# Performance work log

Measured on AMD Instinct MI355X. Metric: run time of the kernel, lower is better.

## Reference

```python
import jax, jax.numpy as jnp
import numpy as np
import math

N_HEAD = 16
N_KV_HEAD = 4
HEAD_DIM = 128
ROTARY_DIM = 128
ROTARY_BASE = 10000
N_CTX = 2048


def _sin_cos(rotary_dim, n_ctx, base):
    pos = np.arange(n_ctx, dtype=np.float32)
    dim = np.arange(rotary_dim // 2, dtype=np.float32)
    freq = base ** (dim / (rotary_dim / 2))
    freq = np.concatenate([freq, freq])  # non-adjacent-pairs layout
    angles = pos[:, None] / freq[None, :]
    return jnp.asarray(np.sin(angles)), jnp.asarray(np.cos(angles))


def _rotate_half(x):
    n = x.shape[-1] // 2
    return jnp.concatenate([-x[..., n:], x[..., :n]], axis=-1)


def setup_inputs() -> dict:
    key = jax.random.key(0)
    ks = jax.random.split(key, 5)
    B, T, C = 2, 2048, 2048
    kv = N_KV_HEAD * HEAD_DIM
    s = 0.02
    return {
        "x": jax.random.normal(ks[0], (B, T, C), jnp.float32),
        "Wq": jax.random.normal(ks[1], (C, C), jnp.float32) * s,
        "Wk": jax.random.normal(ks[2], (kv, C), jnp.float32) * s,
        "Wv": jax.random.normal(ks[3], (kv, C), jnp.float32) * s,
        "Wo": jax.random.normal(ks[4], (C, C), jnp.float32) * s,
    }


def reference(x, Wq, Wk, Wv, Wo):
    B, T, C = x.shape
    q = (x @ Wq.T).reshape(B, T, N_HEAD, HEAD_DIM).transpose(0, 2, 1, 3)    # bhtd
    k = (x @ Wk.T).reshape(B, T, N_KV_HEAD, HEAD_DIM).transpose(0, 2, 1, 3)
    v = (x @ Wv.T).reshape(B, T, N_KV_HEAD, HEAD_DIM).transpose(0, 2, 1, 3)

    sin, cos = _sin_cos(ROTARY_DIM, N_CTX, ROTARY_BASE)
    pos = jnp.arange(T)
    c = cos[pos][None, None, :, :]  # 1,1,T,rot
    s = sin[pos][None, None, :, :]
    q = q * c + _rotate_half(q) * s
    k = k * c + _rotate_half(k) * s

    rep = N_HEAD // N_KV_HEAD
    k = jnp.repeat(k, rep, axis=1)
    v = jnp.repeat(v, rep, axis=1)

    scale = 1.0 / math.sqrt(HEAD_DIM)
    att = jnp.einsum("bhqd,bhkd->bhqk", q, k) * scale
    causal = jnp.tril(jnp.ones((T, T), bool))
    att = jnp.where(causal[None, None], att, -jnp.inf)
    att = jax.nn.softmax(att, axis=-1)
    y = jnp.einsum("bhqk,bhkd->bhqd", att, v)
    y = y.transpose(0, 2, 1, 3).reshape(B, T, C)
    return y @ Wo.T
```

## Files before the change

### kernel.cpp

```cpp
#include <hip/hip_runtime.h>
#include <hip/hip_bf16.h>

typedef float f32x4 __attribute__((ext_vector_type(4)));
typedef float f32x16 __attribute__((ext_vector_type(16)));
typedef short s16x8 __attribute__((ext_vector_type(8)));
typedef short s16x4 __attribute__((ext_vector_type(4)));

__device__ __forceinline__ short f2bf(float f) {
  union { float f; unsigned u; } v; v.f = f;
  unsigned r = v.u + 0x7fffu + ((v.u >> 16) & 1u);
  return (short)(r >> 16);
}
__device__ __forceinline__ float bf2f(short s) {
  union { unsigned u; float f; } v; v.u = ((unsigned)(unsigned short)s) << 16;
  return v.f;
}
__device__ __forceinline__ unsigned cvtpk(float lo, float hi) {
  unsigned r;
  asm("v_cvt_pk_bf16_f32 %0, %1, %2" : "=v"(r) : "v"(lo), "v"(hi));
  return r;
}

__device__ __forceinline__ void gload_lds16(const short* g, short* l) {
  __builtin_amdgcn_global_load_lds(
      (const __attribute__((address_space(1))) void*)g,
      (__attribute__((address_space(3))) void*)l, 16, 0, 0);
}

__global__ __launch_bounds__(256) void k_f2bf(const float* __restrict__ in,
                                              short* __restrict__ out, int n8) {
  int i = blockIdx.x * 256 + threadIdx.x;
  if (i >= n8) return;
  const float4* p = (const float4*)in + (size_t)i * 2;
  float4 a = p[0], b = p[1];
  s16x8 o;
  o[0] = f2bf(a.x); o[1] = f2bf(a.y); o[2] = f2bf(a.z); o[3] = f2bf(a.w);
  o[4] = f2bf(b.x); o[5] = f2bf(b.y); o[6] = f2bf(b.z); o[7] = f2bf(b.w);
  *(s16x8*)(out + (size_t)i * 8) = o;
}

template <int MODE>
__global__ __launch_bounds__(256) void k_gemm_bt(const short* __restrict__ A,
                                                 const short* __restrict__ Bw,
                                                 void* __restrict__ C,
                                                 void* __restrict__ C2,
                                                 void* __restrict__ C3,
                                                 int M, int N, int K) {
  __shared__ __align__(16) short As[128 * 64];
  __shared__ __align__(16) short Bs[128 * 64];
  const int tid = threadIdx.x;
  const int w = tid >> 6, lane = tid & 63;
  const int wm = w >> 1, wn = w & 1;
  const int bm = blockIdx.y, bn = blockIdx.x;
  const int l15 = lane & 15, l4 = lane >> 4;

  f32x4 acc[4][4] = {};

  const int nk = K >> 6;
  for (int kt = 0; kt < nk; ++kt) {
    __syncthreads();
#pragma unroll
    for (int it = 0; it < 4; ++it) {
      int p = it * 256 + tid;
      int p0 = it * 256 + w * 64;
      int r = p >> 3, j = p & 7;
      int jsrc = j ^ (r & 7);
      gload_lds16(A + (size_t)(bm * 128 + r) * K + kt * 64 + jsrc * 8, &As[p0 * 8]);
      gload_lds16(Bw + (size_t)(bn * 128 + r) * K + kt * 64 + jsrc * 8, &Bs[p0 * 8]);
    }
    __syncthreads();
#pragma unroll
    for (int kk = 0; kk < 2; ++kk) {
      s16x8 af[4], bf[4];
      const int jj = kk * 4 + l4;
#pragma unroll
      for (int mi = 0; mi < 4; ++mi) {
        int r = wm * 64 + mi * 16 + l15;
        af[mi] = *(const s16x8*)&As[(r * 8 + (jj ^ (r & 7))) * 8];
      }
#pragma unroll
      for (int ni = 0; ni < 4; ++ni) {
        int r = wn * 64 + ni * 16 + l15;
        bf[ni] = *(const s16x8*)&Bs[(r * 8 + (jj ^ (r & 7))) * 8];
      }
      __builtin_amdgcn_s_setprio(1);
#pragma unroll
      for (int mi = 0; mi < 4; ++mi)
#pragma unroll
        for (int ni = 0; ni < 4; ++ni)
          acc[mi][ni] = __builtin_amdgcn_mfma_f32_16x16x32_bf16(
              af[mi], bf[ni], acc[mi][ni], 0, 0, 0);
      __builtin_amdgcn_s_setprio(0);
    }
  }

#pragma unroll
  for (int mi = 0; mi < 4; ++mi) {
#pragma unroll
    for (int ni = 0; ni < 4; ++ni) {
      int row0 = bm * 128 + wm * 64 + mi * 16 + l4 * 4;
      int col = bn * 128 + wn * 64 + ni * 16 + l15;
      if (MODE == 1) {
        float* Cf = (float*)C;
#pragma unroll
        for (int r2 = 0; r2 < 4; ++r2)
          Cf[(size_t)(row0 + r2) * N + col] = acc[mi][ni][r2];
      } else {
        if (col < 2048) {
          short* Qo = (short*)C;
#pragma unroll
          for (int r2 = 0; r2 < 4; ++r2)
            Qo[(size_t)(row0 + r2) * 2048 + col] = f2bf(acc[mi][ni][r2]);
        } else if (col < 2560) {
          short* Ko = (short*)C2;
#pragma unroll
          for (int r2 = 0; r2 < 4; ++r2)
            Ko[(size_t)(row0 + r2) * 512 + (col - 2048)] = f2bf(acc[mi][ni][r2]);
        } else {
          short* Vo = (short*)C3;
          int b = row0 >> 11, t0 = row0 & 2047;
          s16x4 pk;
#pragma unroll
          for (int r2 = 0; r2 < 4; ++r2) pk[r2] = f2bf(acc[mi][ni][r2]);
          *(s16x4*)&Vo[(size_t)b * 1048576 + (size_t)(col - 2560) * 2048 + t0] = pk;
        }
      }
    }
  }
}

__global__ __launch_bounds__(256) void k_rope(short* __restrict__ X, int shift,
                                              int rowstride, float mul) {
  int idx = blockIdx.x * 256 + threadIdx.x;
  int row = idx >> shift;
  int rem = idx & ((1 << shift) - 1);
  int h = rem >> 6, d = rem & 63;
  int t = row & 2047;
  float inv = exp2f(-(float)d * (13.287712379549449f / 64.f));
  float ang = (float)t * inv;
  float s, c;
  sincosf(ang, &s, &c);
  size_t base = (size_t)row * rowstride + h * 128 + d;
  float q0 = bf2f(X[base]), q1 = bf2f(X[base + 64]);
  X[base] = f2bf((q0 * c - q1 * s) * mul);
  X[base + 64] = f2bf((q1 * c + q0 * s) * mul);
}

__global__ __launch_bounds__(256, 2) void k_attn3(const short* __restrict__ Q,
                                                  const short* __restrict__ Kb,
                                                  const short* __restrict__ Vt,
                                                  short* __restrict__ Y) {
  __shared__ __align__(16) short Ks[2][64 * 128];
  __shared__ __align__(16) short Vs[2][128 * 64];

  const int tid = threadIdx.x;
  const int w = tid >> 6, lane = tid & 63;
  const int l31 = lane & 31, h5 = lane >> 5;
  const int qx = blockIdx.x, h = blockIdx.y, b = blockIdx.z;
  const int qi = b ? (15 - qx) : qx;
  const int kh = h >> 2;

  s16x8 qf[8];
  const int qrow_local = qi * 128 + w * 32 + l31;
  const size_t qrow = (size_t)(b * 2048 + qrow_local);
#pragma unroll
  for (int f = 0; f < 8; ++f)
    qf[f] = *(const s16x8*)(Q + qrow * 2048 + h * 128 + f * 16 + h5 * 8);

  f32x16 oacc[4] = {};
  float m = -1e30f, l = 0.f;

  const int jmax = 2 * qi + 1;

  auto stage = [&](int buf, int j) {
#pragma unroll
    for (int it = 0; it < 4; ++it) {
      int p = it * 256 + tid;
      int p0 = it * 256 + w * 64;
      int r = p >> 4, c = p & 15;
      int csrc = (c - r) & 15;
      gload_lds16(Kb + (size_t)(b * 2048 + j * 64 + r) * 512 + kh * 128 + csrc * 8,
                  &Ks[buf][p0 * 8]);
    }
#pragma unroll
    for (int it = 0; it < 4; ++it) {
      int p = it * 256 + tid;
      int p0 = it * 256 + w * 64;
      int r = p >> 3, c = p & 7;
      int csrc = (c - r) & 7;
      gload_lds16(Vt + (size_t)b * 1048576 + (size_t)(kh * 128 + r) * 2048 +
                      j * 64 + csrc * 8,
                  &Vs[buf][p0 * 8]);
    }
  };

  stage(0, 0);
  __syncthreads();

  for (int j = 0; j <= jmax; ++j) {
    const int cur = j & 1;
    if (j < jmax) stage(cur ^ 1, j + 1);

    f32x16 sa0 = {}, sa1 = {};
    __builtin_amdgcn_s_setprio(1);
#pragma unroll
    for (int f = 0; f < 8; ++f) {
      int c = f * 2 + h5;
      int r0 = l31, r1 = 32 + l31;
      s16x8 k0 = *(const s16x8*)&Ks[cur][(r0 * 16 + ((c + r0) & 15)) * 8];
      s16x8 k1 = *(const s16x8*)&Ks[cur][(r1 * 16 + ((c + r1) & 15)) * 8];
      sa0 = __builtin_amdgcn_mfma_f32_32x32x16_bf16(k0, qf[f], sa0, 0, 0, 0);
      sa1 = __builtin_amdgcn_mfma_f32_32x32x16_bf16(k1, qf[f], sa1, 0, 0, 0);
    }
    __builtin_amdgcn_s_setprio(0);

    if (j >= 2 * qi) {
      const int kv0 = j * 64;
#pragma unroll
      for (int rg = 0; rg < 16; ++rg) {
        int krow = (rg & 3) + 8 * (rg >> 2) + 4 * h5;
        if (kv0 + krow > qrow_local) sa0[rg] = -3.0e38f;
        if (kv0 + 32 + krow > qrow_local) sa1[rg] = -3.0e38f;
      }
    }

    float mx[16];
#pragma unroll
    for (int i = 0; i < 16; ++i) mx[i] = fmaxf(sa0[i], sa1[i]);
#pragma unroll
    for (int stp = 8; stp > 0; stp >>= 1)
#pragma unroll
      for (int i = 0; i < stp; ++i) mx[i] = fmaxf(mx[i], mx[i + stp]);
    float pm = fmaxf(mx[0], __shfl_xor(mx[0], 32));

    if (!__all(pm - m <= 8.f)) {
      float mn = fmaxf(m, pm);
      float al = exp2f(m - mn);
      m = mn;
      l *= al;
#pragma unroll
      for (int d = 0; d < 4; ++d)
#pragma unroll
        for (int i = 0; i < 16; ++i) oacc[d][i] *= al;
    }

    float sm[16];
#pragma unroll
    for (int i = 0; i < 16; ++i) {
      float e0 = exp2f(sa0[i] - m);
      float e1 = exp2f(sa1[i] - m);
      sa0[i] = e0; sa1[i] = e1;
      sm[i] = e0 + e1;
    }
#pragma unroll
    for (int stp = 8; stp > 0; stp >>= 1)
#pragma unroll
      for (int i = 0; i < stp; ++i) sm[i] += sm[i + stp];
    l += sm[0] + __shfl_xor(sm[0], 32);

    unsigned u0[8], u1[8];
#pragma unroll
    for (int g = 0; g < 4; ++g) {
      u0[2 * g]     = cvtpk(sa0[4 * g + 0], sa0[4 * g + 1]);
      u0[2 * g + 1] = cvtpk(sa0[4 * g + 2], sa0[4 * g + 3]);
      u1[2 * g]     = cvtpk(sa1[4 * g + 0], sa1[4 * g + 1]);
      u1[2 * g + 1] = cvtpk(sa1[4 * g + 2], sa1[4 * g + 3]);
    }
    unsigned pu0[8], pu1[8];
#pragma unroll
    for (int g2 = 0; g2 < 8; ++g2) {
      pu0[g2] = __shfl_xor(u0[g2], 32);
      pu1[g2] = __shfl_xor(u1[g2], 32);
    }
    s16x8 pb[4];
#pragma unroll
    for (int fp = 0; fp < 4; ++fp) {
      int j0a = (4 * fp) & 6, j0b = (4 * fp + 2) & 6;
      union { unsigned uu[4]; s16x8 v; } cv;
      if (fp < 2) {
        cv.uu[0] = h5 ? pu0[j0b]     : u0[j0a];
        cv.uu[1] = h5 ? pu0[j0b + 1] : u0[j0a + 1];
        cv.uu[2] = h5 ? u0[j0b]      : pu0[j0a];
        cv.uu[3] = h5 ? u0[j0b + 1]  : pu0[j0a + 1];
      } else {
        cv.uu[0] = h5 ? pu1[j0b]     : u1[j0a];
        cv.uu[1] = h5 ? pu1[j0b + 1] : u1[j0a + 1];
        cv.uu[2] = h5 ? u1[j0b]      : pu1[j0a];
        cv.uu[3] = h5 ? u1[j0b + 1]  : pu1[j0a + 1];
      }
      pb[fp] = cv.v;
    }

    __builtin_amdgcn_s_setprio(1);
#pragma unroll
    for (int dblk = 0; dblk < 4; ++dblk) {
#pragma unroll
      for (int fp = 0; fp < 4; ++fp) {
        int r = dblk * 32 + l31;
        int slot = (fp * 2 + h5 + r) & 7;
        s16x8 vf = *(const s16x8*)&Vs[cur][(r * 8 + slot) * 8];
        oacc[dblk] = __builtin_amdgcn_mfma_f32_32x32x16_bf16(vf, pb[fp],
                                                             oacc[dblk], 0, 0, 0);
      }
    }
    __builtin_amdgcn_s_setprio(0);

    __syncthreads();
  }

  float inv = 1.f / l;
#pragma unroll
  for (int dblk = 0; dblk < 4; ++dblk) {
#pragma unroll
    for (int rg = 0; rg < 4; ++rg) {
      unsigned lo = cvtpk(oacc[dblk][4 * rg + 0] * inv, oacc[dblk][4 * rg + 1] * inv);
      unsigned hi = cvtpk(oacc[dblk][4 * rg + 2] * inv, oacc[dblk][4 * rg + 3] * inv);
      int d0 = dblk * 32 + 8 * rg + 4 * h5;
      uint2 st;
      st.x = lo; st.y = hi;
      *(uint2*)(Y + qrow * 2048 + h * 128 + d0) = st;
    }
  }
}

extern "C" void kernel_launch(void* const* d_in, const int* in_sizes, int n_in,
                              void* d_out, int out_size, void* d_ws, size_t ws_size,
                              hipStream_t stream) {
  (void)in_sizes; (void)n_in; (void)out_size; (void)ws_size;
  const float* x  = (const float*)d_in[0];
  const float* Wq = (const float*)d_in[1];
  const float* Wk = (const float*)d_in[2];
  const float* Wv = (const float*)d_in[3];
  const float* Wo = (const float*)d_in[4];

  char* ws = (char*)d_ws;
  short* xb    = (short*)(ws);
  short* wqkvb = (short*)(ws + 16777216);
  short* wob   = (short*)(ws + 29360128);
  short* Qb    = (short*)(ws + 37748736);
  short* Kb    = (short*)(ws + 54525952);
  short* Vtb   = (short*)(ws + 58720256);
  short* Yb    = (short*)(ws + 62914560);

  k_f2bf<<<4096, 256, 0, stream>>>(x, xb, 1048576);
  k_f2bf<<<2048, 256, 0, stream>>>(Wq, wqkvb, 524288);
  k_f2bf<<<512, 256, 0, stream>>>(Wk, wqkvb + 4194304, 131072);
  k_f2bf<<<512, 256, 0, stream>>>(Wv, wqkvb + 5242880, 131072);
  k_f2bf<<<2048, 256, 0, stream>>>(Wo, wob, 524288);

  k_gemm_bt<3><<<dim3(24, 32), 256, 0, stream>>>(xb, wqkvb, Qb, Kb, Vtb,
                                                 4096, 3072, 2048);

  k_rope<<<16384, 256, 0, stream>>>(Qb, 10, 2048, 0.12751758912141852f);
  k_rope<<<4096, 256, 0, stream>>>(Kb, 8, 512, 1.0f);

  k_attn3<<<dim3(16, 16, 2), 256, 0, stream>>>(Qb, Kb, Vtb, Yb);

  k_gemm_bt<1><<<dim3(16, 32), 256, 0, stream>>>(Yb, wob, d_out, nullptr,
                                                 nullptr, 4096, 2048, 2048);
}
```

Baseline: 211.2 us.

## Merge weight conversions, swizzle GEMM tiles, single-buffer V to raise attention occupancy

The four weight f32→bf16 conversion launches become one kernel, which saves launch overhead. The GEMM now remaps block indices across 8 groups, likely to spread tiles over the XCDs and improve cache locality. The attention kernel drops V's LDS double buffer: V is prefetched into registers and written to a single LDS buffer after each iteration, and launch bounds rise to 3 blocks per CU. This cuts LDS use so occupancy can go up, at the cost of an extra barrier per iteration and more register pressure.

```diff
diff --git a/kernel.cpp b/kernel.cpp
--- a/kernel.cpp
+++ b/kernel.cpp
@@ -37,6 +37,27 @@
   o[0] = f2bf(a.x); o[1] = f2bf(a.y); o[2] = f2bf(a.z); o[3] = f2bf(a.w);
   o[4] = f2bf(b.x); o[5] = f2bf(b.y); o[6] = f2bf(b.z); o[7] = f2bf(b.w);
   *(s16x8*)(out + (size_t)i * 8) = o;
+}
+
+__global__ __launch_bounds__(256) void k_f2bfw(const float* __restrict__ s0,
+                                               const float* __restrict__ s1,
+                                               const float* __restrict__ s2,
+                                               const float* __restrict__ s3,
+                                               short* __restrict__ dqkv,
+                                               short* __restrict__ dwo) {
+  int i = blockIdx.x * 256 + threadIdx.x;
+  const float* src;
+  short* dst;
+  if (i < 524288) { src = s0 + (size_t)i * 8; dst = dqkv + (size_t)i * 8; }
+  else if (i < 655360) { int j = i - 524288; src = s1 + (size_t)j * 8; dst = dqkv + 4194304 + (size_t)j * 8; }
+  else if (i < 786432) { int j = i - 655360; src = s2 + (size_t)j * 8; dst = dqkv + 5242880 + (size_t)j * 8; }
+  else { int j = i - 786432; src = s3 + (size_t)j * 8; dst = dwo + (size_t)j * 8; }
+  const float4* p = (const float4*)src;
+  float4 a = p[0], b = p[1];
+  s16x8 o;
+  o[0] = f2bf(a.x); o[1] = f2bf(a.y); o[2] = f2bf(a.z); o[3] = f2bf(a.w);
+  o[4] = f2bf(b.x); o[5] = f2bf(b.y); o[6] = f2bf(b.z); o[7] = f2bf(b.w);
+  *(s16x8*)dst = o;
 }
 
 template <int MODE>
@@ -51,7 +72,11 @@
   const int tid = threadIdx.x;
   const int w = tid >> 6, lane = tid & 63;
   const int wm = w >> 1, wn = w & 1;
-  const int bm = blockIdx.y, bn = blockIdx.x;
+  const int nbx = gridDim.x;
+  const int f = blockIdx.y * nbx + blockIdx.x;
+  const int cpx = (nbx * gridDim.y) >> 3;
+  const int sw = (f & 7) * cpx + (f >> 3);
+  const int bm = sw / nbx, bn = sw % nbx;
   const int l15 = lane & 15, l4 = lane >> 4;
 
   f32x4 acc[4][4] = {};
@@ -146,12 +171,12 @@
   X[base + 64] = f2bf((q1 * c + q0 * s) * mul);
 }
 
-__global__ __launch_bounds__(256, 2) void k_attn3(const short* __restrict__ Q,
+__global__ __launch_bounds__(256, 3) void k_attn3(const short* __restrict__ Q,
                                                   const short* __restrict__ Kb,
                                                   const short* __restrict__ Vt,
                                                   short* __restrict__ Y) {
   __shared__ __align__(16) short Ks[2][64 * 128];
-  __shared__ __align__(16) short Vs[2][128 * 64];
+  __shared__ __align__(16) short Vs[128 * 64];
 
   const int tid = threadIdx.x;
   const int w = tid >> 6, lane = tid & 63;
@@ -172,7 +197,7 @@
 
   const int jmax = 2 * qi + 1;
 
-  auto stage = [&](int buf, int j) {
+  auto stageK = [&](int buf, int j) {
 #pragma unroll
     for (int it = 0; it < 4; ++it) {
       int p = it * 256 + tid;
@@ -182,24 +207,36 @@
       gload_lds16(Kb + (size_t)(b * 2048 + j * 64 + r) * 512 + kh * 128 + csrc * 8,
                   &Ks[buf][p0 * 8]);
     }
-#pragma unroll
-    for (int it = 0; it < 4; ++it) {
-      int p = it * 256 + tid;
-      int p0 = it * 256 + w * 64;
-      int r = p >> 3, c = p & 7;
-      int csrc = (c - r) & 7;
-      gload_lds16(Vt + (size_t)b * 1048576 + (size_t)(kh * 128 + r) * 2048 +
-                      j * 64 + csrc * 8,
-                  &Vs[buf][p0 * 8]);
-    }
   };
 
-  stage(0, 0);
+  uint4 vreg[4];
+  const int vr0 = tid >> 3, vc0 = tid & 7;
+  const int vslot = (vc0 + vr0) & 7;
+  auto vload = [&](int j) {
+#pragma unroll
+    for (int q = 0; q < 4; ++q) {
+      int r = q * 32 + vr0;
+      vreg[q] = *(const uint4*)(Vt + (size_t)b * 1048576 +
+                                (size_t)(kh * 128 + r) * 2048 + j * 64 + vc0 * 8);
+    }
+  };
+  auto vwrite = [&]() {
+#pragma unroll
+    for (int q = 0; q < 4; ++q) {
+      int r = q * 32 + vr0;
+      *(uint4*)&Vs[(r * 8 + vslot) * 8] = vreg[q];
+    }
+  };
+
+  stageK(0, 0);
+  vload(0);
+  __syncthreads();
+  vwrite();
   __syncthreads();
 
   for (int j = 0; j <= jmax; ++j) {
     const int cur = j & 1;
-    if (j < jmax) stage(cur ^ 1, j + 1);
+    if (j < jmax) { stageK(cur ^ 1, j + 1); vload(j + 1); }
 
     f32x16 sa0 = {}, sa1 = {};
     __builtin_amdgcn_s_setprio(1);
@@ -298,7 +335,7 @@
       for (int fp = 0; fp < 4; ++fp) {
         int r = dblk * 32 + l31;
         int slot = (fp * 2 + h5 + r) & 7;
-        s16x8 vf = *(const s16x8*)&Vs[cur][(r * 8 + slot) * 8];
+        s16x8 vf = *(const s16x8*)&Vs[(r * 8 + slot) * 8];
         oacc[dblk] = __builtin_amdgcn_mfma_f32_32x32x16_bf16(vf, pb[fp],
                                                              oacc[dblk], 0, 0, 0);
       }
@@ -306,6 +343,10 @@
     __builtin_amdgcn_s_setprio(0);
 
     __syncthreads();
+    if (j < jmax) {
+      vwrite();
+      __syncthreads();
+    }
   }
 
   float inv = 1.f / l;
@@ -343,10 +384,7 @@
   short* Yb    = (short*)(ws + 62914560);
 
   k_f2bf<<<4096, 256, 0, stream>>>(x, xb, 1048576);
-  k_f2bf<<<2048, 256, 0, stream>>>(Wq, wqkvb, 524288);
-  k_f2bf<<<512, 256, 0, stream>>>(Wk, wqkvb + 4194304, 131072);
-  k_f2bf<<<512, 256, 0, stream>>>(Wv, wqkvb + 5242880, 131072);
-  k_f2bf<<<2048, 256, 0, stream>>>(Wo, wob, 524288);
+  k_f2bfw<<<5120, 256, 0, stream>>>(Wq, Wk, Wv, Wo, wqkvb, wob);
 
   k_gemm_bt<3><<<dim3(24, 32), 256, 0, stream>>>(xb, wqkvb, Qb, Kb, Vtb,
                                                  4096, 3072, 2048);
```

Result: slower. 327.8 us (+55.2%).
